# Optimization experiments

Measured on AMD Instinct MI355X. Metric: run time of the kernel, lower is better.

## Reference

```python
import jax, jax.numpy as jnp
import numpy as np


def setup_inputs() -> dict:
    key = jax.random.key(0)
    k1, k2, k3, k4 = jax.random.split(key, 4)
    B, S, dAR, dEnc, K, N = 32, 128, 256, 256, 12, 128
    W = S - K  # windowSize = 116
    cFeature = jax.random.normal(k1, (B, S, dAR), dtype=jnp.float32)
    encodedData = jax.random.normal(k2, (B, S, dEnc), dtype=jnp.float32)
    Wp = jax.random.normal(k3, (K, dEnc, dAR), dtype=jnp.float32) * 0.05
    extIdx = jax.random.randint(k4, (N * W * B,), 0, B * S, dtype=jnp.int64)
    return {"cFeature": cFeature, "encodedData": encodedData, "Wp": Wp, "extIdx": extIdx}


def reference(cFeature, encodedData, Wp, extIdx):
    B, S, dAR = cFeature.shape
    K = Wp.shape[0]                      # nPredicts
    e = encodedData.shape[-1]            # dimOutputEncoder
    W = S - K                            # windowSize
    N = extIdx.shape[0] // (B * W)       # negativeSamplingExt

    c = cFeature[:, :W]                                          # (B, W, dAR)
    # negative sampling: flat gather then reshape, as in sample()
    negExt = encodedData.reshape(-1, e)[extIdx].reshape(B, N, W, e)

    # all predictor Linears at once: locC[k] = c @ Wp[k].T -> (K, B, W, e)
    locC = jnp.einsum('bwa,kea->kbwe', c, Wp)

    # positive sequences: encodedData[:, k+1 : k+1+W] for each predictor k
    pos = jnp.stack([encodedData[:, k + 1:k + 1 + W] for k in range(K)])  # (K,B,W,e)

    inv_e = 1.0 / e  # (locC * cand).mean(dim=3)
    posScore = jnp.einsum('kbwe,kbwe->kbw', locC, pos) * inv_e            # (K,B,W)
    negScore = jnp.einsum('kbwe,bnwe->kbnw', locC, negExt) * inv_e        # (K,B,N,W)

    logits = jnp.concatenate([posScore[:, :, None, :], negScore], axis=2)  # (K,B,1+N,W)
    logits = jnp.transpose(logits, (0, 1, 3, 2)).reshape(K, B * W, 1 + N)

    # cross-entropy with label 0 (positive is class 0), mean over B*W samples
    lse = jax.nn.logsumexp(logits, axis=-1)                                # (K, B*W)
    losses = jnp.mean(lse - logits[..., 0], axis=-1)                       # (K,)
    acc = jnp.mean((jnp.argmax(logits, axis=-1) == 0).astype(jnp.float32), axis=-1)
    return losses[None, :], acc[None, :]
```

## Files before the change

kernel.cpp:

```cpp
#include <hip/hip_runtime.h>

#define HD __device__ __forceinline__

typedef __attribute__((ext_vector_type(4))) float f32x4;
typedef __attribute__((ext_vector_type(8))) short bf16x8;
typedef __attribute__((ext_vector_type(2))) long i64x2;

constexpr int B_ = 32, S_ = 128, DA = 256, DE = 256, K_ = 12, N_ = 128;
constexpr int W_ = S_ - K_;
constexpr int BW = B_ * W_;

HD unsigned short f2bf(float f) {
    unsigned u = __float_as_uint(f);
    u += 0x7fffu + ((u >> 16) & 1u);
    return (unsigned short)(u >> 16);
}

__global__ void k_prep(const float* __restrict__ A, const float* __restrict__ Wp,
                       const float* __restrict__ E, const int* __restrict__ idx,
                       unsigned short* __restrict__ Abf, unsigned short* __restrict__ Wpbf,
                       unsigned char* __restrict__ Ebf8, unsigned short* __restrict__ idxT) {
    int bx = blockIdx.x;
    if (bx < 1792) {
        const float* src = (bx < 1024) ? A : Wp;
        unsigned short* dst = (bx < 1024) ? Abf : Wpbf;
        int base = (bx < 1024) ? bx : bx - 1024;
        int i = base * 256 + threadIdx.x;
        float4 v = ((const float4*)src)[i];
        ushort4 o;
        o.x = f2bf(v.x); o.y = f2bf(v.y); o.z = f2bf(v.z); o.w = f2bf(v.w);
        ((ushort4*)dst)[i] = o;
    } else if (bx < 2816) {
        int i = (bx - 1792) * 256 + threadIdx.x;
        float4 v = ((const float4*)E)[i];
        int w = __builtin_amdgcn_cvt_pk_fp8_f32(v.x, v.y, 0, false);
        w     = __builtin_amdgcn_cvt_pk_fp8_f32(v.z, v.w, w, true);
        ((unsigned int*)Ebf8)[i] = w;
    } else {
        __shared__ unsigned short lt[W_][130];
        int b = bx - 2816;
        const int* ib = idx + b * N_ * W_;
        for (int i = threadIdx.x; i < N_ * W_; i += 256) {
            int n = i / W_, w = i - n * W_;
            lt[w][n] = (unsigned short)ib[i];
        }
        __syncthreads();
        unsigned short* ob = idxT + b * W_ * N_;
        for (int o = threadIdx.x; o < W_ * N_; o += 256) {
            int w = o >> 7, n = o & 127;
            ob[o] = lt[w][n];
        }
    }
}

__global__ __launch_bounds__(256) void k_locc(const unsigned short* __restrict__ Abf,
                                              const unsigned short* __restrict__ Wpbf,
                                              unsigned char* __restrict__ locC8) {
    int bx = blockIdx.x;
    int k  = bx / 58;
    int r  = bx % 58;
    int mt = r >> 1;
    int et = r & 1;

    __shared__ unsigned short As[128][40];
    __shared__ unsigned short Bs[128][40];

    int tid  = threadIdx.x;
    int lane = tid & 63;
    int wid  = tid >> 6;
    int wr   = wid >> 1, wc = wid & 1;
    int l15  = lane & 15, lk = lane >> 4;

    f32x4 acc[4][4] = {};

    int srow = tid >> 1, spart = tid & 1;
    int m  = mt * 128 + srow;
    int bb = m / W_, ww = m - bb * W_;
    const unsigned short* aSrc = Abf + ((bb * S_ + ww) * DA) + spart * 16;
    const unsigned short* bSrc = Wpbf + ((k * DE + et * 128 + srow) * DA) + spart * 16;

    for (int c = 0; c < 8; ++c) {
        uint4 av0 = ((const uint4*)(aSrc + c * 32))[0];
        uint4 av1 = ((const uint4*)(aSrc + c * 32))[1];
        uint4 bv0 = ((const uint4*)(bSrc + c * 32))[0];
        uint4 bv1 = ((const uint4*)(bSrc + c * 32))[1];
        __syncthreads();
        ((uint4*)&As[srow][spart * 16])[0]     = av0;
        ((uint4*)&As[srow][spart * 16 + 8])[0] = av1;
        ((uint4*)&Bs[srow][spart * 16])[0]     = bv0;
        ((uint4*)&Bs[srow][spart * 16 + 8])[0] = bv1;
        __syncthreads();
        bf16x8 af[4], bfv[4];
        #pragma unroll
        for (int f = 0; f < 4; ++f) {
            af[f]  = *(const bf16x8*)&As[wc * 64 + f * 16 + l15][lk * 8];
            bfv[f] = *(const bf16x8*)&Bs[wr * 64 + f * 16 + l15][lk * 8];
        }
        #pragma unroll
        for (int fi = 0; fi < 4; ++fi)
            #pragma unroll
            for (int fj = 0; fj < 4; ++fj)
                acc[fi][fj] = __builtin_amdgcn_mfma_f32_16x16x32_bf16(bfv[fi], af[fj], acc[fi][fj], 0, 0, 0);
    }

    #pragma unroll
    for (int fi = 0; fi < 4; ++fi) {
        #pragma unroll
        for (int fj = 0; fj < 4; ++fj) {
            f32x4 v = acc[fi][fj];
            int mOut  = mt * 128 + wc * 64 + fj * 16 + l15;
            int eBase = et * 128 + wr * 64 + fi * 16 + lk * 4;
            int w = __builtin_amdgcn_cvt_pk_fp8_f32(v[0], v[1], 0, false);
            w     = __builtin_amdgcn_cvt_pk_fp8_f32(v[2], v[3], w, true);
            *(unsigned int*)(locC8 + (size_t)mOut * (K_ * DE) + k * DE + eBase) = w;
        }
    }
}

__global__ __launch_bounds__(256, 2) void k_score(const unsigned char* __restrict__ Ebf8,
                                                  const unsigned short* __restrict__ idxT,
                                                  const unsigned char* __restrict__ locC8,
                                                  float* __restrict__ partial) {
    int tid  = threadIdx.x;
    int lane = tid & 63;
    int wid  = tid >> 6;
    int l15  = lane & 15, lk = lane >> 4;
    int p    = blockIdx.x * 4 + wid;
    int b    = p / W_, w = p - b * W_;

    int rows[9];
    #pragma unroll
    for (int nf = 0; nf < 8; ++nf)
        rows[nf] = idxT[p * N_ + nf * 16 + l15];
    rows[8] = b * S_ + ((l15 < K_) ? (w + l15 + 1) : 0);

    i64x2 af[4];
    const unsigned char* aBase = locC8 + (size_t)p * (K_ * DE) + l15 * DE + lk * 16;
    #pragma unroll
    for (int c = 0; c < 4; ++c) {
        i64x2 a = {};
        if (l15 < K_) a = *(const i64x2*)(aBase + c * 64);
        af[c] = a;
    }

    i64x2 bv[9][4];
    #pragma unroll
    for (int nf = 0; nf < 9; ++nf) {
        const unsigned char* bBase = Ebf8 + (size_t)rows[nf] * DE + lk * 16;
        #pragma unroll
        for (int c = 0; c < 4; ++c)
            bv[nf][c] = *(const i64x2*)(bBase + c * 64);
    }

    f32x4 accs[9];
    #pragma unroll
    for (int nf = 0; nf < 9; ++nf) {
        f32x4 acc = {};
        #pragma unroll
        for (int c = 0; c < 4; ++c) {
            acc = __builtin_amdgcn_mfma_f32_16x16x32_fp8_fp8(af[c][0], bv[nf][c][0], acc, 0, 0, 0);
            acc = __builtin_amdgcn_mfma_f32_16x16x32_fp8_fp8(af[c][1], bv[nf][c][1], acc, 0, 0, 0);
        }
        accs[nf] = acc;
    }

    constexpr float inv_e = 1.0f / 256.0f;

    float m0[4], s0[4];
    #pragma unroll
    for (int rr = 0; rr < 4; ++rr) {
        float mx = accs[0][rr];
        #pragma unroll
        for (int nf = 1; nf < 8; ++nf) mx = fmaxf(mx, accs[nf][rr]);
        m0[rr] = mx;
    }
    #pragma unroll
    for (int off = 1; off < 16; off <<= 1)
        #pragma unroll
        for (int rr = 0; rr < 4; ++rr) m0[rr] = fmaxf(m0[rr], __shfl_xor(m0[rr], off));

    #pragma unroll
    for (int rr = 0; rr < 4; ++rr) {
        float s = 0.f;
        #pragma unroll
        for (int nf = 0; nf < 8; ++nf) s += __expf((accs[nf][rr] - m0[rr]) * inv_e);
        s0[rr] = s;
    }
    #pragma unroll
    for (int off = 1; off < 16; off <<= 1)
        #pragma unroll
        for (int rr = 0; rr < 4; ++rr) s0[rr] += __shfl_xor(s0[rr], off);

    if (l15 < K_ && lk == (l15 >> 2)) {
        int k = l15;
        #pragma unroll
        for (int rr = 0; rr < 4; ++rr) {
            if ((k & 3) == rr) {
                float ps   = accs[8][rr] * inv_e;
                float mneg = m0[rr] * inv_e;
                float M    = fmaxf(mneg, ps);
                float tot  = s0[rr] * __expf(mneg - M) + __expf(ps - M);
                partial[k * BW + p]        = M + __logf(tot) - ps;
                partial[(12 + k) * BW + p] = (ps >= mneg) ? 1.0f : 0.0f;
            }
        }
    }
}

__global__ void k_reduce(const float* __restrict__ partial, float* __restrict__ out) {
    int o = blockIdx.x;
    float s = 0.f;
    for (int i = threadIdx.x; i < BW; i += 256) s += partial[o * BW + i];
    #pragma unroll
    for (int off = 32; off > 0; off >>= 1) s += __shfl_xor(s, off);
    __shared__ float w4[4];
    if ((threadIdx.x & 63) == 0) w4[threadIdx.x >> 6] = s;
    __syncthreads();
    if (threadIdx.x == 0)
        out[o] = (w4[0] + w4[1] + w4[2] + w4[3]) * (1.0f / BW);
}

extern "C" void kernel_launch(void* const* d_in, const int* in_sizes, int n_in,
                              void* d_out, int out_size, void* d_ws, size_t ws_size,
                              hipStream_t stream) {
    const float* cFeat = (const float*)d_in[0];
    const float* E     = (const float*)d_in[1];
    const float* Wp    = (const float*)d_in[2];
    const int*   idx   = (const int*)d_in[3];

    char* ws = (char*)d_ws;
    unsigned char*  locC8   = (unsigned char*) (ws);
    unsigned short* Abf     = (unsigned short*)(ws + 22806528);
    unsigned short* Wpbf    = (unsigned short*)(ws + 24903680);
    float*          partial = (float*)        (ws + 26476544);
    unsigned char*  Ebf8    = (unsigned char*) (ws + 26833024);
    unsigned short* idxT    = (unsigned short*)(ws + 27881600);

    k_prep<<<2816 + 32, 256, 0, stream>>>(cFeat, Wp, E, idx, Abf, Wpbf, Ebf8, idxT);
    k_locc<<<12 * 58, 256, 0, stream>>>(Abf, Wpbf, locC8);
    k_score<<<BW / 4, 256, 0, stream>>>(Ebf8, idxT, locC8, partial);
    k_reduce<<<24, 256, 0, stream>>>(partial, (float*)d_out);
}
```

Baseline: 113.3 us.

## Fuse loss reduction into score kernel via atomics and use direct global-to-LDS loads

Replaces the separate reduction kernel with block-level shared-memory atomics in the score kernel followed by global atomics into the output, which is zeroed in the prep kernel. The locC GEMM now stages tiles with global_load_lds directly into unpadded LDS instead of going through registers. This removes one kernel launch and the partial buffer traffic, and cuts register staging. In exchange, summation order becomes nondeterministic and the unpadded LDS may add bank conflicts.

```diff
diff --git a/kernel.cpp b/kernel.cpp
--- a/kernel.cpp
+++ b/kernel.cpp
@@ -16,10 +16,17 @@
     return (unsigned short)(u >> 16);
 }
 
+HD void gl2lds16(const void* g, void* l) {
+    __builtin_amdgcn_global_load_lds(
+        (const __attribute__((address_space(1))) unsigned int*)g,
+        (__attribute__((address_space(3))) unsigned int*)l, 16, 0, 0);
+}
+
 __global__ void k_prep(const float* __restrict__ A, const float* __restrict__ Wp,
                        const float* __restrict__ E, const int* __restrict__ idx,
                        unsigned short* __restrict__ Abf, unsigned short* __restrict__ Wpbf,
-                       unsigned char* __restrict__ Ebf8, unsigned short* __restrict__ idxT) {
+                       unsigned char* __restrict__ Ebf8, unsigned short* __restrict__ idxT,
+                       float* __restrict__ dout) {
     int bx = blockIdx.x;
     if (bx < 1792) {
         const float* src = (bx < 1024) ? A : Wp;
@@ -36,7 +43,7 @@
         int w = __builtin_amdgcn_cvt_pk_fp8_f32(v.x, v.y, 0, false);
         w     = __builtin_amdgcn_cvt_pk_fp8_f32(v.z, v.w, w, true);
         ((unsigned int*)Ebf8)[i] = w;
-    } else {
+    } else if (bx < 2848) {
         __shared__ unsigned short lt[W_][130];
         int b = bx - 2816;
         const int* ib = idx + b * N_ * W_;
@@ -50,51 +57,57 @@
             int w = o >> 7, n = o & 127;
             ob[o] = lt[w][n];
         }
+    } else {
+        if (threadIdx.x < 24) dout[threadIdx.x] = 0.f;
     }
 }
 
 __global__ __launch_bounds__(256) void k_locc(const unsigned short* __restrict__ Abf,
                                               const unsigned short* __restrict__ Wpbf,
                                               unsigned char* __restrict__ locC8) {
+    __shared__ unsigned short As[128 * 32];
+    __shared__ unsigned short Bs[128 * 32];
+
     int bx = blockIdx.x;
     int k  = bx / 58;
     int r  = bx % 58;
     int mt = r >> 1;
     int et = r & 1;
 
-    __shared__ unsigned short As[128][40];
-    __shared__ unsigned short Bs[128][40];
-
     int tid  = threadIdx.x;
     int lane = tid & 63;
     int wid  = tid >> 6;
     int wr   = wid >> 1, wc = wid & 1;
     int l15  = lane & 15, lk = lane >> 4;
 
+    int m0 = mt * 128 + wid * 32 + (lane >> 2);
+    int m1 = m0 + 16;
+    int b0 = m0 / W_, w0 = m0 - b0 * W_;
+    int b1 = m1 / W_, w1 = m1 - b1 * W_;
+    const unsigned short* aS0 = Abf + (size_t)(b0 * S_ + w0) * DA + (lane & 3) * 8;
+    const unsigned short* aS1 = Abf + (size_t)(b1 * S_ + w1) * DA + (lane & 3) * 8;
+    int e0 = et * 128 + wid * 32 + (lane >> 2);
+    const unsigned short* bS0 = Wpbf + (size_t)(k * DE + e0) * DA + (lane & 3) * 8;
+    const unsigned short* bS1 = bS0 + 16 * DA;
+    unsigned short* aD0 = As + (wid * 32) * 32;
+    unsigned short* aD1 = As + (wid * 32 + 16) * 32;
+    unsigned short* bD0 = Bs + (wid * 32) * 32;
+    unsigned short* bD1 = Bs + (wid * 32 + 16) * 32;
+
     f32x4 acc[4][4] = {};
 
-    int srow = tid >> 1, spart = tid & 1;
-    int m  = mt * 128 + srow;
-    int bb = m / W_, ww = m - bb * W_;
-    const unsigned short* aSrc = Abf + ((bb * S_ + ww) * DA) + spart * 16;
-    const unsigned short* bSrc = Wpbf + ((k * DE + et * 128 + srow) * DA) + spart * 16;
-
     for (int c = 0; c < 8; ++c) {
-        uint4 av0 = ((const uint4*)(aSrc + c * 32))[0];
-        uint4 av1 = ((const uint4*)(aSrc + c * 32))[1];
-        uint4 bv0 = ((const uint4*)(bSrc + c * 32))[0];
-        uint4 bv1 = ((const uint4*)(bSrc + c * 32))[1];
         __syncthreads();
-        ((uint4*)&As[srow][spart * 16])[0]     = av0;
-        ((uint4*)&As[srow][spart * 16 + 8])[0] = av1;
-        ((uint4*)&Bs[srow][spart * 16])[0]     = bv0;
-        ((uint4*)&Bs[srow][spart * 16 + 8])[0] = bv1;
+        gl2lds16(aS0 + c * 32, aD0);
+        gl2lds16(aS1 + c * 32, aD1);
+        gl2lds16(bS0 + c * 32, bD0);
+        gl2lds16(bS1 + c * 32, bD1);
         __syncthreads();
         bf16x8 af[4], bfv[4];
         #pragma unroll
         for (int f = 0; f < 4; ++f) {
-            af[f]  = *(const bf16x8*)&As[wc * 64 + f * 16 + l15][lk * 8];
-            bfv[f] = *(const bf16x8*)&Bs[wr * 64 + f * 16 + l15][lk * 8];
+            af[f]  = *(const bf16x8*)&As[(wc * 64 + f * 16 + l15) * 32 + lk * 8];
+            bfv[f] = *(const bf16x8*)&Bs[(wr * 64 + f * 16 + l15) * 32 + lk * 8];
         }
         #pragma unroll
         for (int fi = 0; fi < 4; ++fi)
@@ -120,7 +133,9 @@
 __global__ __launch_bounds__(256, 2) void k_score(const unsigned char* __restrict__ Ebf8,
                                                   const unsigned short* __restrict__ idxT,
                                                   const unsigned char* __restrict__ locC8,
-                                                  float* __restrict__ partial) {
+                                                  float* __restrict__ dout) {
+    __shared__ float sacc[24];
+
     int tid  = threadIdx.x;
     int lane = tid & 63;
     int wid  = tid >> 6;
@@ -128,6 +143,9 @@
     int p    = blockIdx.x * 4 + wid;
     int b    = p / W_, w = p - b * W_;
 
+    if (tid < 24) sacc[tid] = 0.f;
+    __syncthreads();
+
     int rows[9];
     #pragma unroll
     for (int nf = 0; nf < 8; ++nf)
@@ -165,6 +183,7 @@
     }
 
     constexpr float inv_e = 1.0f / 256.0f;
+    constexpr float inv_bw = 1.0f / BW;
 
     float m0[4], s0[4];
     #pragma unroll
@@ -200,24 +219,13 @@
                 float mneg = m0[rr] * inv_e;
                 float M    = fmaxf(mneg, ps);
                 float tot  = s0[rr] * __expf(mneg - M) + __expf(ps - M);
-                partial[k * BW + p]        = M + __logf(tot) - ps;
-                partial[(12 + k) * BW + p] = (ps >= mneg) ? 1.0f : 0.0f;
+                atomicAdd(&sacc[k],      (M + __logf(tot) - ps) * inv_bw);
+                atomicAdd(&sacc[12 + k], (ps >= mneg) ? inv_bw : 0.0f);
             }
         }
     }
-}
-
-__global__ void k_reduce(const float* __restrict__ partial, float* __restrict__ out) {
-    int o = blockIdx.x;
-    float s = 0.f;
-    for (int i = threadIdx.x; i < BW; i += 256) s += partial[o * BW + i];
-    #pragma unroll
-    for (int off = 32; off > 0; off >>= 1) s += __shfl_xor(s, off);
-    __shared__ float w4[4];
-    if ((threadIdx.x & 63) == 0) w4[threadIdx.x >> 6] = s;
     __syncthreads();
-    if (threadIdx.x == 0)
-        out[o] = (w4[0] + w4[1] + w4[2] + w4[3]) * (1.0f / BW);
+    if (tid < 24) atomicAdd(&dout[tid], sacc[tid]);
 }
 
 extern "C" void kernel_launch(void* const* d_in, const int* in_sizes, int n_in,
@@ -232,12 +240,11 @@
     unsigned char*  locC8   = (unsigned char*) (ws);
     unsigned short* Abf     = (unsigned short*)(ws + 22806528);
     unsigned short* Wpbf    = (unsigned short*)(ws + 24903680);
-    float*          partial = (float*)        (ws + 26476544);
     unsigned char*  Ebf8    = (unsigned char*) (ws + 26833024);
     unsigned short* idxT    = (unsigned short*)(ws + 27881600);
-
-    k_prep<<<2816 + 32, 256, 0, stream>>>(cFeat, Wp, E, idx, Abf, Wpbf, Ebf8, idxT);
+    float*          dout    = (float*)d_out;
+
+    k_prep<<<2849, 256, 0, stream>>>(cFeat, Wp, E, idx, Abf, Wpbf, Ebf8, idxT, dout);
     k_locc<<<12 * 58, 256, 0, stream>>>(Abf, Wpbf, locC8);
-    k_score<<<BW / 4, 256, 0, stream>>>(Ebf8, idxT, locC8, partial);
-    k_reduce<<<24, 256, 0, stream>>>(partial, (float*)d_out);
-}
+    k_score<<<BW / 4, 256, 0, stream>>>(Ebf8, idxT, locC8, dout);
+}
```

After: 111.9 us. No clear change (-1.2%).
